# Performance work log

Hardware: AMD Instinct MI355X
Metric: run time of the kernel (lower is better)

## Reference

```python
import jax, jax.numpy as jnp
import numpy as np

B, S, D = 4, 2048, 1024
H = 16
DH = D // H  # dim_q = dim_k = 64
F = 4096
EPS = 1e-5


def setup_inputs() -> dict:
    key = jax.random.key(0)
    ks = jax.random.split(key, 16)
    sd = 0.02
    inp = {
        'x': jax.random.normal(ks[0], (B, S, D), jnp.float32),
        'wq': jax.random.normal(ks[1], (H, D, DH), jnp.float32) * sd,
        'bq': jnp.zeros((H, DH), jnp.float32),
        'wk': jax.random.normal(ks[2], (H, D, DH), jnp.float32) * sd,
        'bk': jnp.zeros((H, DH), jnp.float32),
        'wv': jax.random.normal(ks[3], (H, D, DH), jnp.float32) * sd,
        'bv': jnp.zeros((H, DH), jnp.float32),
        'wo': jax.random.normal(ks[4], (H * DH, D), jnp.float32) * sd,
        'bo': jnp.zeros((D,), jnp.float32),
        'ln1_g': jnp.ones((D,), jnp.float32),
        'ln1_b': jnp.zeros((D,), jnp.float32),
        'w1': jax.random.normal(ks[5], (D, F), jnp.float32) * sd,
        'b1': jnp.zeros((F,), jnp.float32),
        'w2': jax.random.normal(ks[6], (F, D), jnp.float32) * sd,
        'b2': jnp.zeros((D,), jnp.float32),
        'ln2_g': jnp.ones((D,), jnp.float32),
        'ln2_b': jnp.zeros((D,), jnp.float32),
    }
    return inp


def _layernorm(x, g, b):
    mu = jnp.mean(x, axis=-1, keepdims=True)
    var = jnp.mean(jnp.square(x - mu), axis=-1, keepdims=True)
    return (x - mu) * jax.lax.rsqrt(var + EPS) * g + b


def _encoder_layer(x, wq, bq, wk, bk, wv, bv, wo, bo, ln1_g, ln1_b,
                   w1, b1, w2, b2, ln2_g, ln2_b):
    # Multi-head attention (all heads batched via einsum)
    q = jnp.einsum('bsd,hde->bhse', x, wq) + bq[:, None, :]
    k = jnp.einsum('bsd,hde->bhse', x, wk) + bk[:, None, :]
    v = jnp.einsum('bsd,hde->bhse', x, wv) + bv[:, None, :]
    scores = jnp.einsum('bhqe,bhke->bhqk', q, k) / jnp.sqrt(jnp.float32(DH))
    p = jax.nn.softmax(scores, axis=-1)
    o = jnp.einsum('bhqk,bhke->bhqe', p, v)  # [B,H,S,DH]
    o = o.transpose(0, 2, 1, 3).reshape(B, S, H * DH)  # concat heads
    attn = o @ wo + bo
    y = _layernorm(x + attn, ln1_g, ln1_b)  # post-norm residual
    # Feed-forward
    ff = jax.nn.relu(y @ w1 + b1) @ w2 + b2
    return _layernorm(y + ff, ln2_g, ln2_b)


def reference(x, wq, bq, wk, bk, wv, bv, wo, bo, ln1_g, ln1_b,
              w1, b1, w2, b2, ln2_g, ln2_b):
    return _encoder_layer(x, wq, bq, wk, bk, wv, bv, wo, bo, ln1_g, ln1_b,
                          w1, b1, w2, b2, ln2_g, ln2_b)
```

## Files before the change

kernel.cpp:

```cpp
#include <hip/hip_runtime.h>
#include <stdint.h>


typedef short bf16x8 __attribute__((ext_vector_type(8)));
typedef unsigned short u16x8 __attribute__((ext_vector_type(8)));
typedef float f32x4 __attribute__((ext_vector_type(4)));
typedef unsigned int u32x2 __attribute__((ext_vector_type(2)));

#define MFMA16(a, b, c) __builtin_amdgcn_mfma_f32_16x16x32_bf16((a), (b), (c), 0, 0, 0)

#define QSCALE 0.1803368801111204f

__device__ __forceinline__ float b2f(unsigned short u) {
    union { unsigned u32; float f; } x;
    x.u32 = ((unsigned)u) << 16;
    return x.f;
}
__device__ __forceinline__ unsigned short f2b(float f) {
    union { float f; unsigned u; } x;
    x.f = f;
    unsigned r = x.u + 0x7fff + ((x.u >> 16) & 1);
    return (unsigned short)(r >> 16);
}

__device__ __forceinline__ void gl16(const unsigned short* g, unsigned short* l) {
    __builtin_amdgcn_global_load_lds(
        (__attribute__((address_space(1))) unsigned int*)(unsigned long)g,
        (__attribute__((address_space(3))) unsigned int*)l, 16, 0, 0);
}

__global__ __launch_bounds__(256) void f2b_bulk(const float* __restrict__ in,
                                                unsigned short* __restrict__ out) {
    const long i = ((long)blockIdx.x * 256 + threadIdx.x) * 8;
    float4 a = *(const float4*)&in[i];
    float4 b = *(const float4*)&in[i + 4];
    u16x8 u;
    u[0] = f2b(a.x); u[1] = f2b(a.y); u[2] = f2b(a.z); u[3] = f2b(a.w);
    u[4] = f2b(b.x); u[5] = f2b(b.y); u[6] = f2b(b.z); u[7] = f2b(b.w);
    *(u16x8*)&out[i] = u;
}

__global__ void transpose_f2b(const float* __restrict__ in,
                              unsigned short* __restrict__ out,
                              int R, int C, long in_batch_stride,
                              int out_row0, int out_ld) {
    __shared__ float tile[32][33];
    const int batch = blockIdx.z;
    const float* src = in + (long)batch * in_batch_stride;
    const int c0 = blockIdx.x * 32, r0 = blockIdx.y * 32;
    const int tx = threadIdx.x, ty = threadIdx.y;
#pragma unroll
    for (int i = 0; i < 32; i += 8)
        tile[ty + i][tx] = src[(long)(r0 + ty + i) * C + c0 + tx];
    __syncthreads();
#pragma unroll
    for (int i = 0; i < 32; i += 8)
        out[(long)(out_row0 + batch * C + c0 + ty + i) * out_ld + r0 + tx] =
            f2b(tile[tx][ty + i]);
}

__global__ void transpose_v(const unsigned short* __restrict__ qkv,
                            unsigned short* __restrict__ vt) {
    __shared__ unsigned short tile[32][33];
    const int bh = blockIdx.z;
    const int b = bh >> 4, h = bh & 15;
    const int s0 = blockIdx.x * 32, e0 = blockIdx.y * 32;
    const int tx = threadIdx.x, ty = threadIdx.y;
    const unsigned short* src = qkv + ((long)b * 2048) * 3072 + 2048 + h * 64;
#pragma unroll
    for (int i = 0; i < 32; i += 8)
        tile[ty + i][tx] = src[(long)(s0 + ty + i) * 3072 + e0 + tx];
    __syncthreads();
    unsigned short* dst = vt + ((long)bh * 64) * 2048;
#pragma unroll
    for (int i = 0; i < 32; i += 8)
        dst[(long)(e0 + ty + i) * 2048 + s0 + tx] = tile[tx][ty + i];
}

__global__ void concat_bias(const float* __restrict__ bq,
                            const float* __restrict__ bk,
                            const float* __restrict__ bv,
                            float* __restrict__ out) {
    int n = blockIdx.x * 256 + threadIdx.x;
    out[n] = (n < 1024) ? bq[n] : (n < 2048) ? bk[n - 1024] : bv[n - 2048];
}

__device__ __forceinline__ float to_f(float v) { return v; }
__device__ __forceinline__ float to_f(unsigned short v) { return b2f(v); }

template <typename RT>
__global__ __launch_bounds__(512, 2) void gemm_ring(
    const unsigned short* __restrict__ A, const unsigned short* __restrict__ Bt,
    unsigned short* __restrict__ C, const float* __restrict__ bias,
    const RT* __restrict__ resid, int M, int N, int K, int op) {
    __shared__ __align__(16) unsigned short As[4][256 * 32];
    __shared__ __align__(16) unsigned short Bs[4][128 * 32];
    const int tid = threadIdx.x;
    const int wave = tid >> 6, lane = tid & 63;
    const int quad = lane >> 4, lr = lane & 15;
    const int wm = wave >> 1, wn = wave & 1;

    const int nwg = gridDim.x * gridDim.y;
    const int orig = blockIdx.y * gridDim.x + blockIdx.x;
    const int wg = (orig & 7) * (nwg >> 3) + (orig >> 3);
    const long n0 = (long)(wg % gridDim.x) * 128;
    const long m0 = (long)(wg / gridDim.x) * 256;

    f32x4 acc[4][4] = {};

    const unsigned short* gA =
        A + (m0 + wave * 32 + (lane >> 2)) * (long)K + (lane & 3) * 8;
    const unsigned short* gB =
        Bt + (n0 + wave * 16 + (lane >> 2)) * (long)K + (lane & 3) * 8;
    const long rstep = 16 * (long)K;
    unsigned short* const lA0 = &As[0][wave * 32 * 32];
    unsigned short* const lA1 = &As[0][(wave * 32 + 16) * 32];
    unsigned short* const lB0 = &Bs[0][wave * 16 * 32];

#define RSTAGE(si)                                                  \
    {                                                               \
        const int _sl = (si) & 3;                                   \
        const long _kc = (long)(si) * 32;                           \
        gl16(gA + _kc, lA0 + _sl * 8192);                           \
        gl16(gA + rstep + _kc, lA1 + _sl * 8192);                   \
        gl16(gB + _kc, lB0 + _sl * 4096);                           \
    }

    const int S = K >> 5;
    RSTAGE(0);
    RSTAGE(1);
    RSTAGE(2);

    for (int s = 0; s < S; ++s) {
        if (s + 2 < S) {
            asm volatile("s_waitcnt vmcnt(6)" ::: "memory");
        } else if (s + 1 < S) {
            asm volatile("s_waitcnt vmcnt(3)" ::: "memory");
        } else {
            asm volatile("s_waitcnt vmcnt(0)" ::: "memory");
        }
        __builtin_amdgcn_s_barrier();
        const int slot = s & 3;
        bf16x8 af[4], bfr[4];
#pragma unroll
        for (int mi = 0; mi < 4; mi++)
            af[mi] = *(const bf16x8*)&As[slot][(wm * 64 + mi * 16 + lr) * 32 + quad * 8];
#pragma unroll
        for (int ni = 0; ni < 4; ni++)
            bfr[ni] = *(const bf16x8*)&Bs[slot][(wn * 64 + ni * 16 + lr) * 32 + quad * 8];
#pragma unroll
        for (int mi = 0; mi < 4; mi++)
#pragma unroll
            for (int ni = 0; ni < 4; ni++)
                acc[mi][ni] = MFMA16(af[mi], bfr[ni], acc[mi][ni]);
        if (s + 3 < S) RSTAGE(s + 3);
    }
#undef RSTAGE

#pragma unroll
    for (int ni = 0; ni < 4; ni++) {
        const long col = n0 + wn * 64 + ni * 16 + lr;
        const float bv = bias ? bias[col] : 0.0f;
        const float cscale = (op == 2 && col < 1024) ? QSCALE : 1.0f;
#pragma unroll
        for (int mi = 0; mi < 4; mi++) {
#pragma unroll
            for (int r = 0; r < 4; r++) {
                const long row = m0 + wm * 64 + mi * 16 + quad * 4 + r;
                float v = (acc[mi][ni][r] + bv) * cscale;
                if (resid) v += to_f(resid[row * (long)N + col]);
                if (op == 1) v = fmaxf(v, 0.0f);
                C[row * (long)N + col] = f2b(v);
            }
        }
    }
}

__global__ __launch_bounds__(256, 5) void attn_kernel(
    const unsigned short* __restrict__ qkv, const unsigned short* __restrict__ vt,
    unsigned short* __restrict__ o) {
    __shared__ __align__(16) unsigned short Klds[2][64 * 64];
    __shared__ __align__(16) unsigned short Vlds[2][64 * 64];
    const int l = blockIdx.x;
    const int bh = ((l >> 8) << 3) | (l & 7);
    const int qt = (l >> 3) & 31;
    const int b = bh >> 4, h = bh & 15;
    const int tid = threadIdx.x;
    const int wave = tid >> 6, lane = tid & 63;
    const int quad = lane >> 4, lr = lane & 15;
    const long rowbase = (long)b * 2048;
    const int qb = qt * 64 + wave * 16;

    bf16x8 q0, q1;
    {
        const unsigned short* qrow = qkv + (rowbase + qb + lr) * 3072 + h * 64;
        q0 = *(const bf16x8*)&qrow[quad * 8];
        q1 = *(const bf16x8*)&qrow[32 + quad * 8];
    }

    bf16x8 ones;
#pragma unroll
    for (int i = 0; i < 8; i++) ones[i] = (short)0x3F80;

    const int srow = lane >> 3;
    const int sxc = (lane & 7) ^ srow;
    const unsigned short* kp =
        qkv + (rowbase + wave * 16 + srow) * 3072 + 1024 + h * 64 + sxc * 8;
    const unsigned short* vp =
        vt + ((long)bh * 64 + wave * 16 + srow) * 2048 + sxc * 8;
    const long KADV = 64L * 3072;
    unsigned short* const kd0 = &Klds[0][wave * 16 * 64];
    unsigned short* const vd0 = &Vlds[0][wave * 16 * 64];

#define STAGE(bf)                                                     \
    {                                                                 \
        gl16(kp, kd0 + (bf)*4096);                                    \
        gl16(kp + 8 * 3072, kd0 + (bf)*4096 + 8 * 64);                \
        gl16(vp, vd0 + (bf)*4096);                                    \
        gl16(vp + 8 * 2048, vd0 + (bf)*4096 + 8 * 64);                \
    }

    f32x4 oacc[4] = {};
    f32x4 dacc = {};

    const int x7 = lr & 7;
    const int c00 = (quad ^ x7) * 8;
    const int c01 = ((4 | quad) ^ x7) * 8;

    STAGE(0);
    __syncthreads();

    for (int kt = 0; kt < 32; kt++) {
        const int buf = kt & 1;
        if (kt < 31) {
            kp += KADV;
            vp += 64;
            STAGE(buf ^ 1);
        }
        const unsigned short* kb = &Klds[buf][0];
        f32x4 s4[4];
#pragma unroll
        for (int nt = 0; nt < 4; nt++) {
            const unsigned short* krow = kb + (nt * 16 + lr) * 64;
            bf16x8 k0 = *(const bf16x8*)&krow[c00];
            bf16x8 k1 = *(const bf16x8*)&krow[c01];
            f32x4 z = {};
            z = MFMA16(k0, q0, z);
            z = MFMA16(k1, q1, z);
            s4[nt] = z;
        }
        unsigned pwv[4][2];
#pragma unroll
        for (int nt = 0; nt < 4; nt++) {
            float p0 = exp2f(s4[nt][0]);
            float p1 = exp2f(s4[nt][1]);
            float p2 = exp2f(s4[nt][2]);
            float p3 = exp2f(s4[nt][3]);
            asm("v_cvt_pk_bf16_f32 %0, %1, %2"
                : "=v"(pwv[nt][0]) : "v"(p0), "v"(p1));
            asm("v_cvt_pk_bf16_f32 %0, %1, %2"
                : "=v"(pwv[nt][1]) : "v"(p2), "v"(p3));
        }
        unsigned pq[2][4];
#pragma unroll
        for (int kc = 0; kc < 2; kc++)
#pragma unroll
            for (int tl = 0; tl < 2; tl++) {
                u32x2 y = __builtin_amdgcn_permlane32_swap(
                    pwv[2 * kc][tl], pwv[2 * kc + 1][tl], false, false);
                u32x2 z = __builtin_amdgcn_permlane16_swap(y[0], y[1], false, false);
                pq[kc][tl] = z[0];
                pq[kc][2 + tl] = z[1];
            }

        const unsigned short* vb = &Vlds[buf][0];
#pragma unroll
        for (int kc = 0; kc < 2; kc++) {
            union { unsigned u[4]; bf16x8 h; } pu;
            pu.u[0] = pq[kc][0]; pu.u[1] = pq[kc][1];
            pu.u[2] = pq[kc][2]; pu.u[3] = pq[kc][3];
            const int vc = kc ? c01 : c00;
            dacc = MFMA16(ones, pu.h, dacc);
#pragma unroll
            for (int nt = 0; nt < 4; nt++) {
                bf16x8 va = *(const bf16x8*)&vb[(nt * 16 + lr) * 64 + vc];
                oacc[nt] = MFMA16(va, pu.h, oacc[nt]);
            }
        }
        __syncthreads();
    }

    const float rinv = 1.0f / dacc[0];

    const long orow = rowbase + qb + lr;
#pragma unroll
    for (int nt = 0; nt < 4; nt++) {
        ushort4 ov = {f2b(oacc[nt][0] * rinv), f2b(oacc[nt][1] * rinv),
                      f2b(oacc[nt][2] * rinv), f2b(oacc[nt][3] * rinv)};
        *(ushort4*)&o[orow * 1024 + h * 64 + nt * 16 + quad * 4] = ov;
    }
#undef STAGE
}

__device__ __forceinline__ void st4(float* p, float a, float b, float c, float d) {
    float4 v = {a, b, c, d};
    *(float4*)p = v;
}
__device__ __forceinline__ void st4(unsigned short* p, float a, float b, float c,
                                    float d) {
    ushort4 v = {f2b(a), f2b(b), f2b(c), f2b(d)};
    *(ushort4*)p = v;
}

template <typename OT>
__global__ __launch_bounds__(256) void ln_kernel(
    const unsigned short* __restrict__ in, const float* __restrict__ g,
    const float* __restrict__ b, OT* __restrict__ out) {
    __shared__ float red[4];
    const long row = blockIdx.x;
    const int tid = threadIdx.x;
    ushort4 u = *(const ushort4*)&in[row * 1024 + tid * 4];
    float v[4] = {b2f(u.x), b2f(u.y), b2f(u.z), b2f(u.w)};
    float s = v[0] + v[1] + v[2] + v[3];
#pragma unroll
    for (int off = 32; off > 0; off >>= 1) s += __shfl_down(s, off, 64);
    if ((tid & 63) == 0) red[tid >> 6] = s;
    __syncthreads();
    const float mu = (red[0] + red[1] + red[2] + red[3]) * (1.0f / 1024.0f);
    __syncthreads();
    float d[4], sq = 0.f;
#pragma unroll
    for (int i = 0; i < 4; i++) { d[i] = v[i] - mu; sq += d[i] * d[i]; }
#pragma unroll
    for (int off = 32; off > 0; off >>= 1) sq += __shfl_down(sq, off, 64);
    if ((tid & 63) == 0) red[tid >> 6] = sq;
    __syncthreads();
    const float var = (red[0] + red[1] + red[2] + red[3]) * (1.0f / 1024.0f);
    const float rs = rsqrtf(var + 1e-5f);
    float4 gu = *(const float4*)&g[tid * 4];
    float4 bu = *(const float4*)&b[tid * 4];
    st4(&out[row * 1024 + tid * 4], d[0] * rs * gu.x + bu.x,
        d[1] * rs * gu.y + bu.y, d[2] * rs * gu.z + bu.z,
        d[3] * rs * gu.w + bu.w);
}

extern "C" void kernel_launch(void* const* d_in, const int* in_sizes, int n_in,
                              void* d_out, int out_size, void* d_ws, size_t ws_size,
                              hipStream_t stream) {
    (void)in_sizes; (void)n_in; (void)out_size; (void)ws_size;
    const float* x   = (const float*)d_in[0];
    const float* wq  = (const float*)d_in[1];
    const float* bq  = (const float*)d_in[2];
    const float* wk  = (const float*)d_in[3];
    const float* bk  = (const float*)d_in[4];
    const float* wv  = (const float*)d_in[5];
    const float* bv  = (const float*)d_in[6];
    const float* wo  = (const float*)d_in[7];
    const float* bo  = (const float*)d_in[8];
    const float* g1  = (const float*)d_in[9];
    const float* be1 = (const float*)d_in[10];
    const float* w1  = (const float*)d_in[11];
    const float* b1  = (const float*)d_in[12];
    const float* w2  = (const float*)d_in[13];
    const float* b2  = (const float*)d_in[14];
    const float* g2  = (const float*)d_in[15];
    const float* be2 = (const float*)d_in[16];

    char* ws = (char*)d_ws;
    const size_t MB = 1024 * 1024;
    unsigned short* WT_QKV = (unsigned short*)(ws + 0);
    unsigned short* WT_O   = (unsigned short*)(ws + 6 * MB);
    unsigned short* WT_1   = (unsigned short*)(ws + 8 * MB);
    unsigned short* WT_2   = (unsigned short*)(ws + 16 * MB);
    float*          BQKV   = (float*)(ws + 24 * MB);
    unsigned short* XB     = (unsigned short*)(ws + 25 * MB);
    unsigned short* QKV    = (unsigned short*)(ws + 41 * MB);
    unsigned short* O      = (unsigned short*)(ws + 89 * MB);
    unsigned short* R1     = (unsigned short*)(ws + 25 * MB);
    unsigned short* Y      = (unsigned short*)(ws + 41 * MB);
    unsigned short* R2     = (unsigned short*)(ws + 57 * MB);
    unsigned short* Hb     = (unsigned short*)(ws + 73 * MB);
    unsigned short* VT     = (unsigned short*)(ws + 137 * MB);
    float*          OUT    = (float*)d_out;

    const dim3 tb(32, 8, 1);
    transpose_f2b<<<dim3(2, 32, 16), tb, 0, stream>>>(wq, WT_QKV, 1024, 64, 65536L, 0, 1024);
    transpose_f2b<<<dim3(2, 32, 16), tb, 0, stream>>>(wk, WT_QKV, 1024, 64, 65536L, 1024, 1024);
    transpose_f2b<<<dim3(2, 32, 16), tb, 0, stream>>>(wv, WT_QKV, 1024, 64, 65536L, 2048, 1024);
    transpose_f2b<<<dim3(32, 32, 1), tb, 0, stream>>>(wo, WT_O, 1024, 1024, 0L, 0, 1024);
    transpose_f2b<<<dim3(128, 32, 1), tb, 0, stream>>>(w1, WT_1, 1024, 4096, 0L, 0, 1024);
    transpose_f2b<<<dim3(32, 128, 1), tb, 0, stream>>>(w2, WT_2, 4096, 1024, 0L, 0, 4096);
    concat_bias<<<dim3(12), 256, 0, stream>>>(bq, bk, bv, BQKV);
    f2b_bulk<<<dim3(4096), 256, 0, stream>>>(x, XB);

    gemm_ring<unsigned short><<<dim3(24, 32), 512, 0, stream>>>(
        XB, WT_QKV, QKV, BQKV, (const unsigned short*)nullptr, 8192, 3072, 1024, 2);
    transpose_v<<<dim3(64, 2, 64), tb, 0, stream>>>(QKV, VT);
    attn_kernel<<<dim3(2048), 256, 0, stream>>>(QKV, VT, O);
    gemm_ring<float><<<dim3(8, 32), 512, 0, stream>>>(
        O, WT_O, R1, bo, x, 8192, 1024, 1024, 0);
    ln_kernel<unsigned short><<<dim3(8192), 256, 0, stream>>>(R1, g1, be1, Y);
    gemm_ring<unsigned short><<<dim3(32, 32), 512, 0, stream>>>(
        Y, WT_1, Hb, b1, (const unsigned short*)nullptr, 8192, 4096, 1024, 1);
    gemm_ring<unsigned short><<<dim3(8, 32), 512, 0, stream>>>(
        Hb, WT_2, R2, b2, Y, 8192, 1024, 4096, 0);
    ln_kernel<float><<<dim3(8192), 256, 0, stream>>>(R2, g2, be2, OUT);
}
```

Before: 613.4 us.

## Restructure GEMM into 8-phase interleaved load/MFMA schedule with swizzled LDS

Replaces the ring-buffered GEMM with a version that uses 128x256 tiles in place of 256x128, lays the 8 waves out as 2x4, and applies an XOR swizzle to LDS chunks to reduce bank conflicts. Each K-step is split into four MFMA phases, with LDS fragment reads and global prefetch loads interleaved between them. The phases are separated by barriers and s_setprio so compute and memory traffic overlap in a ping-pong pattern across waves. This adds many more barriers per iteration and a more fragile waitcnt schedule.

```diff
diff --git a/kernel.cpp b/kernel.cpp
--- a/kernel.cpp
+++ b/kernel.cpp
@@ -89,84 +89,146 @@
 __device__ __forceinline__ float to_f(unsigned short v) { return b2f(v); }
 
 template <typename RT>
-__global__ __launch_bounds__(512, 2) void gemm_ring(
+__global__ __launch_bounds__(512, 2) void gemm8p(
     const unsigned short* __restrict__ A, const unsigned short* __restrict__ Bt,
     unsigned short* __restrict__ C, const float* __restrict__ bias,
     const RT* __restrict__ resid, int M, int N, int K, int op) {
-    __shared__ __align__(16) unsigned short As[4][256 * 32];
-    __shared__ __align__(16) unsigned short Bs[4][128 * 32];
+    __shared__ __align__(16) unsigned short As[4][128 * 32];
+    __shared__ __align__(16) unsigned short Bs[4][256 * 32];
     const int tid = threadIdx.x;
-    const int wave = tid >> 6, lane = tid & 63;
+    const int lane = tid & 63;
+    const int wave = tid >> 6;
     const int quad = lane >> 4, lr = lane & 15;
-    const int wm = wave >> 1, wn = wave & 1;
-
-    const int nwg = gridDim.x * gridDim.y;
-    const int orig = blockIdx.y * gridDim.x + blockIdx.x;
+    const int wr = wave >> 2, wc = wave & 3;
+
+    const int nx = gridDim.x;
+    const int nwg = nx * gridDim.y;
+    const int orig = blockIdx.y * nx + blockIdx.x;
     const int wg = (orig & 7) * (nwg >> 3) + (orig >> 3);
-    const long n0 = (long)(wg % gridDim.x) * 128;
-    const long m0 = (long)(wg / gridDim.x) * 256;
+    const long n0 = (long)(wg % nx) * 256;
+    const long m0 = (long)(wg / nx) * 128;
 
     f32x4 acc[4][4] = {};
 
-    const unsigned short* gA =
-        A + (m0 + wave * 32 + (lane >> 2)) * (long)K + (lane & 3) * 8;
-    const unsigned short* gB =
-        Bt + (n0 + wave * 16 + (lane >> 2)) * (long)K + (lane & 3) * 8;
-    const long rstep = 16 * (long)K;
-    unsigned short* const lA0 = &As[0][wave * 32 * 32];
-    unsigned short* const lA1 = &As[0][(wave * 32 + 16) * 32];
-    unsigned short* const lB0 = &Bs[0][wave * 16 * 32];
-
-#define RSTAGE(si)                                                  \
-    {                                                               \
-        const int _sl = (si) & 3;                                   \
-        const long _kc = (long)(si) * 32;                           \
-        gl16(gA + _kc, lA0 + _sl * 8192);                           \
-        gl16(gA + rstep + _kc, lA1 + _sl * 8192);                   \
-        gl16(gB + _kc, lB0 + _sl * 4096);                           \
+    const int trow = tid >> 2;
+    const int tch = ((tid & 3) ^ ((tid >> 3) & 3)) * 8;
+    const unsigned short* gA0 = A + (m0 + trow) * (long)K + tch;
+    const unsigned short* gB0 = Bt + (n0 + trow) * (long)K + tch;
+    const unsigned short* gB1 = Bt + (n0 + 128 + trow) * (long)K + tch;
+    unsigned short* const dA = &As[0][0] + tid * 8;
+    unsigned short* const dB = &Bs[0][0] + tid * 8;
+
+    int aoff[4], boff[4];
+#pragma unroll
+    for (int mi = 0; mi < 4; mi++) {
+        const int r = wr * 64 + mi * 16 + lr;
+        aoff[mi] = r * 32 + (quad ^ ((r >> 1) & 3)) * 8;
+    }
+#pragma unroll
+    for (int ni = 0; ni < 4; ni++) {
+        const int r = wc * 64 + ni * 16 + lr;
+        boff[ni] = r * 32 + (quad ^ ((r >> 1) & 3)) * 8;
+    }
+
+#define G8_STAGE(si, u)                                                   \
+    {                                                                     \
+        if ((u) == 0)                                                     \
+            gl16(gA0 + (long)(si) * 32, dA + ((si) & 3) * 4096);          \
+        else if ((u) == 1)                                                \
+            gl16(gB0 + (long)(si) * 32, dB + ((si) & 3) * 8192);          \
+        else                                                              \
+            gl16(gB1 + (long)(si) * 32, dB + ((si) & 3) * 8192 + 4096);   \
     }
 
     const int S = K >> 5;
-    RSTAGE(0);
-    RSTAGE(1);
-    RSTAGE(2);
+    for (int s = 0; s < 3; s++) {
+        G8_STAGE(s, 0);
+        G8_STAGE(s, 1);
+        G8_STAGE(s, 2);
+    }
+    asm volatile("s_waitcnt vmcnt(6)" ::: "memory");
+    __builtin_amdgcn_s_barrier();
 
     for (int s = 0; s < S; ++s) {
-        if (s + 2 < S) {
+        const int slot = s & 3;
+        const unsigned short* as_ = &As[slot][0];
+        const unsigned short* bs_ = &Bs[slot][0];
+        const bool st = (s + 3) < S;
+        bf16x8 af0[2], af1[2], bf0[2], bf1[2];
+        af0[0] = *(const bf16x8*)&as_[aoff[0]];
+        af0[1] = *(const bf16x8*)&as_[aoff[1]];
+        bf0[0] = *(const bf16x8*)&bs_[boff[0]];
+        bf0[1] = *(const bf16x8*)&bs_[boff[1]];
+        if (st) G8_STAGE(s + 3, 0);
+        __builtin_amdgcn_s_barrier();
+        asm volatile("s_waitcnt lgkmcnt(0)" ::: "memory");
+        __builtin_amdgcn_sched_barrier(0);
+        __builtin_amdgcn_s_setprio(1);
+        acc[0][0] = MFMA16(af0[0], bf0[0], acc[0][0]);
+        acc[0][1] = MFMA16(af0[0], bf0[1], acc[0][1]);
+        acc[1][0] = MFMA16(af0[1], bf0[0], acc[1][0]);
+        acc[1][1] = MFMA16(af0[1], bf0[1], acc[1][1]);
+        __builtin_amdgcn_s_setprio(0);
+        __builtin_amdgcn_s_barrier();
+        __builtin_amdgcn_sched_barrier(0);
+        bf1[0] = *(const bf16x8*)&bs_[boff[2]];
+        bf1[1] = *(const bf16x8*)&bs_[boff[3]];
+        if (st) G8_STAGE(s + 3, 1);
+        __builtin_amdgcn_s_barrier();
+        asm volatile("s_waitcnt lgkmcnt(0)" ::: "memory");
+        __builtin_amdgcn_sched_barrier(0);
+        __builtin_amdgcn_s_setprio(1);
+        acc[0][2] = MFMA16(af0[0], bf1[0], acc[0][2]);
+        acc[0][3] = MFMA16(af0[0], bf1[1], acc[0][3]);
+        acc[1][2] = MFMA16(af0[1], bf1[0], acc[1][2]);
+        acc[1][3] = MFMA16(af0[1], bf1[1], acc[1][3]);
+        __builtin_amdgcn_s_setprio(0);
+        __builtin_amdgcn_s_barrier();
+        __builtin_amdgcn_sched_barrier(0);
+        af1[0] = *(const bf16x8*)&as_[aoff[2]];
+        af1[1] = *(const bf16x8*)&as_[aoff[3]];
+        if (st) G8_STAGE(s + 3, 2);
+        __builtin_amdgcn_s_barrier();
+        asm volatile("s_waitcnt lgkmcnt(0)" ::: "memory");
+        __builtin_amdgcn_sched_barrier(0);
+        __builtin_amdgcn_s_setprio(1);
+        acc[2][2] = MFMA16(af1[0], bf1[0], acc[2][2]);
+        acc[2][3] = MFMA16(af1[0], bf1[1], acc[2][3]);
+        acc[3][2] = MFMA16(af1[1], bf1[0], acc[3][2]);
+        acc[3][3] = MFMA16(af1[1], bf1[1], acc[3][3]);
+        __builtin_amdgcn_s_setprio(0);
+        __builtin_amdgcn_s_barrier();
+        __builtin_amdgcn_sched_barrier(0);
+        if (s + 3 < S) {
             asm volatile("s_waitcnt vmcnt(6)" ::: "memory");
-        } else if (s + 1 < S) {
+        } else if (s + 2 < S) {
             asm volatile("s_waitcnt vmcnt(3)" ::: "memory");
         } else {
             asm volatile("s_waitcnt vmcnt(0)" ::: "memory");
         }
         __builtin_amdgcn_s_barrier();
-        const int slot = s & 3;
-        bf16x8 af[4], bfr[4];
-#pragma unroll
-        for (int mi = 0; mi < 4; mi++)
-            af[mi] = *(const bf16x8*)&As[slot][(wm * 64 + mi * 16 + lr) * 32 + quad * 8];
-#pragma unroll
-        for (int ni = 0; ni < 4; ni++)
-            bfr[ni] = *(const bf16x8*)&Bs[slot][(wn * 64 + ni * 16 + lr) * 32 + quad * 8];
-#pragma unroll
-        for (int mi = 0; mi < 4; mi++)
-#pragma unroll
-            for (int ni = 0; ni < 4; ni++)
-                acc[mi][ni] = MFMA16(af[mi], bfr[ni], acc[mi][ni]);
-        if (s + 3 < S) RSTAGE(s + 3);
-    }
-#undef RSTAGE
+        __builtin_amdgcn_sched_barrier(0);
+        __builtin_amdgcn_s_setprio(1);
+        acc[2][0] = MFMA16(af1[0], bf0[0], acc[2][0]);
+        acc[2][1] = MFMA16(af1[0], bf0[1], acc[2][1]);
+        acc[3][0] = MFMA16(af1[1], bf0[0], acc[3][0]);
+        acc[3][1] = MFMA16(af1[1], bf0[1], acc[3][1]);
+        __builtin_amdgcn_s_setprio(0);
+        __builtin_amdgcn_s_barrier();
+        __builtin_amdgcn_sched_barrier(0);
+    }
+#undef G8_STAGE
 
 #pragma unroll
     for (int ni = 0; ni < 4; ni++) {
-        const long col = n0 + wn * 64 + ni * 16 + lr;
+        const long col = n0 + wc * 64 + ni * 16 + lr;
         const float bv = bias ? bias[col] : 0.0f;
         const float cscale = (op == 2 && col < 1024) ? QSCALE : 1.0f;
 #pragma unroll
         for (int mi = 0; mi < 4; mi++) {
 #pragma unroll
             for (int r = 0; r < 4; r++) {
-                const long row = m0 + wm * 64 + mi * 16 + quad * 4 + r;
+                const long row = m0 + wr * 64 + mi * 16 + quad * 4 + r;
                 float v = (acc[mi][ni][r] + bv) * cscale;
                 if (resid) v += to_f(resid[row * (long)N + col]);
                 if (op == 1) v = fmaxf(v, 0.0f);
@@ -393,16 +455,16 @@
     concat_bias<<<dim3(12), 256, 0, stream>>>(bq, bk, bv, BQKV);
     f2b_bulk<<<dim3(4096), 256, 0, stream>>>(x, XB);
 
-    gemm_ring<unsigned short><<<dim3(24, 32), 512, 0, stream>>>(
+    gemm8p<unsigned short><<<dim3(12, 64), 512, 0, stream>>>(
         XB, WT_QKV, QKV, BQKV, (const unsigned short*)nullptr, 8192, 3072, 1024, 2);
     transpose_v<<<dim3(64, 2, 64), tb, 0, stream>>>(QKV, VT);
     attn_kernel<<<dim3(2048), 256, 0, stream>>>(QKV, VT, O);
-    gemm_ring<float><<<dim3(8, 32), 512, 0, stream>>>(
+    gemm8p<float><<<dim3(4, 64), 512, 0, stream>>>(
         O, WT_O, R1, bo, x, 8192, 1024, 1024, 0);
     ln_kernel<unsigned short><<<dim3(8192), 256, 0, stream>>>(R1, g1, be1, Y);
-    gemm_ring<unsigned short><<<dim3(32, 32), 512, 0, stream>>>(
+    gemm8p<unsigned short><<<dim3(16, 64), 512, 0, stream>>>(
         Y, WT_1, Hb, b1, (const unsigned short*)nullptr, 8192, 4096, 1024, 1);
-    gemm_ring<unsigned short><<<dim3(8, 32), 512, 0, stream>>>(
+    gemm8p<unsigned short><<<dim3(4, 64), 512, 0, stream>>>(
         Hb, WT_2, R2, b2, Y, 8192, 1024, 4096, 0);
     ln_kernel<float><<<dim3(8192), 256, 0, stream>>>(R2, g2, be2, OUT);
 }
```

After: 652.8 us. 6.4% more time.
